# Kernel optimization log

Hardware: AMD Instinct MI355X
Metric: run time of the kernel (lower is better)

Reference implementation:

```python
import jax, jax.numpy as jnp
import numpy as np

EPS = 0.1
TANH_SCALE = 1.0
B, T, N, D, C, DE = 8, 120, 24, 48, 1128, 256  # C = D*(D-1)//2


def setup_inputs() -> dict:
    key = jax.random.key(0)
    k1, k2, k3, k4 = jax.random.split(key, 4)
    x = jax.random.normal(k1, (B, T, N, D), dtype=jnp.float32)
    context = jax.random.normal(k2, (B, C, N, DE), dtype=jnp.float32)
    Wkv = jax.random.normal(k3, (D, DE), dtype=jnp.float32) * (DE ** -0.5)
    bkv = jax.random.normal(k4, (D,), dtype=jnp.float32) * 0.01
    return {"x": x, "context": context, "Wkv": Wkv, "bkv": bkv}


def reference(x, context, Wkv, bkv):
    # x: [B,T,N,D], context: [B,C,N,DE]
    b, t, n, d = x.shape
    kv = jnp.einsum('bcne,de->bcnd', context, Wkv) + bkv      # [B,C,N,D]
    kv = jnp.transpose(kv, (0, 2, 3, 1))                      # [B,N,D,C]
    xt = jnp.transpose(x, (0, 2, 1, 3))                       # [B,N,T,D]
    sp = jnp.einsum('bntd,bndc->bntc', xt, kv)                # [B,N,T,C]
    sp = EPS * TANH_SCALE * jnp.tanh(sp / TANH_SCALE)
    i, j = jnp.tril_indices(d, k=-1)
    A = jnp.zeros((b, n, t, d, d), dtype=x.dtype).at[..., i, j].set(sp)
    A = A - jnp.swapaxes(A, -1, -2)                           # skew-symmetric
    dx = jnp.einsum('bntd,bntde->bnte', xt, A)                # per-(B,N,T) matvec
    y = xt + dx
    return jnp.transpose(y, (0, 2, 1, 3))                     # [B,T,N,D]
```

## Files before the change

kernel.cpp:

```cpp
#include <hip/hip_runtime.h>


constexpr int Bc = 8, Tc = 120, Nc = 24, Dc = 48, Cc = 1128, DEc = 256;
constexpr int BNc = Bc * Nc;
constexpr int KVP = 64;

using short8 = __attribute__((ext_vector_type(8))) short;
using f32x4  = __attribute__((ext_vector_type(4))) float;

__device__ __forceinline__ ushort f2b(float f) {
    union { float f; unsigned u; } v; v.f = f;
    unsigned r = (v.u + 0x7fffu + ((v.u >> 16) & 1u)) >> 16;
    return (ushort)r;
}
__device__ __forceinline__ short8 pack8(const float4& a, const float4& b) {
    short8 r;
    r[0] = (short)f2b(a.x); r[1] = (short)f2b(a.y); r[2] = (short)f2b(a.z); r[3] = (short)f2b(a.w);
    r[4] = (short)f2b(b.x); r[5] = (short)f2b(b.y); r[6] = (short)f2b(b.z); r[7] = (short)f2b(b.w);
    return r;
}

constexpr int SWs = 264;
constexpr int STs = 72;
__global__ __launch_bounds__(256) void k1_kv(const float* __restrict__ ctx,
                                             const float* __restrict__ Wkv,
                                             const float* __restrict__ bkv,
                                             ushort* __restrict__ kvb) {
    __shared__ ushort sW[Dc * SWs];
    __shared__ ushort sT[4][32 * STs];
    const int bn = blockIdx.x, c0 = blockIdx.y * 128;
    const int b = bn / Nc, n = bn % Nc;
    const int tid = threadIdx.x, wave = tid >> 6, lane = tid & 63;
    const int tr = lane & 15, kg = lane >> 4;
    const float* ctxb = ctx + ((size_t)b * Cc * Nc + n) * DEc;

    for (int l = tid; l < Dc * 64; l += 256) {
        int d = l >> 6, e4 = (l & 63) << 2;
        float4 w = *reinterpret_cast<const float4*>(Wkv + d * DEc + e4);
        ushort4 u = make_ushort4(f2b(w.x), f2b(w.y), f2b(w.z), f2b(w.w));
        *reinterpret_cast<ushort4*>(&sW[d * SWs + e4]) = u;
    }
    __syncthreads();

    const float* arow[2];
    #pragma unroll
    for (int mf = 0; mf < 2; ++mf) {
        int c = c0 + wave * 32 + mf * 16 + tr;
        arow[mf] = ctxb + (size_t)(c < Cc ? c : Cc - 1) * (Nc * DEc);
    }

    f32x4 acc[2][3];
    #pragma unroll
    for (int mf = 0; mf < 2; ++mf)
        #pragma unroll
        for (int nf = 0; nf < 3; ++nf) acc[mf][nf] = (f32x4){0.f, 0.f, 0.f, 0.f};

    #pragma unroll
    for (int ks = 0; ks < 8; ++ks) {
        const int e0 = ks * 32 + kg * 8;
        short8 af[2];
        #pragma unroll
        for (int mf = 0; mf < 2; ++mf) {
            float4 a0 = *reinterpret_cast<const float4*>(arow[mf] + e0);
            float4 a1 = *reinterpret_cast<const float4*>(arow[mf] + e0 + 4);
            af[mf] = pack8(a0, a1);
        }
        short8 bf[3];
        #pragma unroll
        for (int nf = 0; nf < 3; ++nf)
            bf[nf] = *reinterpret_cast<const short8*>(&sW[(nf * 16 + tr) * SWs + ks * 32 + kg * 8]);
        #pragma unroll
        for (int mf = 0; mf < 2; ++mf)
            #pragma unroll
            for (int nf = 0; nf < 3; ++nf)
                acc[mf][nf] = __builtin_amdgcn_mfma_f32_16x16x32_bf16(af[mf], bf[nf], acc[mf][nf], 0, 0, 0);
    }

    float bias[3];
    #pragma unroll
    for (int nf = 0; nf < 3; ++nf) bias[nf] = bkv[nf * 16 + tr];
    #pragma unroll
    for (int mf = 0; mf < 2; ++mf)
        #pragma unroll
        for (int nf = 0; nf < 3; ++nf)
            #pragma unroll
            for (int r = 0; r < 4; ++r)
                sT[wave][(mf * 16 + kg * 4 + r) * STs + nf * 16 + tr] = f2b(acc[mf][nf][r] + bias[nf]);
    {
        int row = lane >> 1, half = lane & 1;
        short8 z = (short8){0, 0, 0, 0, 0, 0, 0, 0};
        *reinterpret_cast<short8*>(&sT[wave][row * STs + 48 + half * 8]) = z;
    }
    __syncthreads();
    #pragma unroll
    for (int p = 0; p < 4; ++p) {
        int row = p * 8 + (lane >> 3), colv = (lane & 7) * 8;
        short8 v = *reinterpret_cast<const short8*>(&sT[wave][row * STs + colv]);
        int c = c0 + wave * 32 + row;
        if (c < Cc)
            *reinterpret_cast<short8*>(&kvb[((size_t)bn * Cc + c) * KVP + colv]) = v;
    }
}

constexpr int SGs = 1136;
__global__ __launch_bounds__(256) void k2_fused(const float* __restrict__ x,
                                                const ushort* __restrict__ kvb,
                                                float* __restrict__ out) {
    __shared__ float  sG[16 * SGs];
    __shared__ float  sXf[16 * 52];
    __shared__ ushort sXb[16 * 72];
    const int L = blockIdx.x;
    const int bn = (L & 7) + 8 * (L >> 6);
    const int tt = (L >> 3) & 7;
    const int b = bn / Nc, n = bn % Nc, t0 = tt * 16;
    const int tid = threadIdx.x, wave = tid >> 6, lane = tid & 63;
    const int tr = lane & 15, kg = lane >> 4;

    for (int l = tid; l < 16 * 72 / 4; l += 256)
        *reinterpret_cast<ushort4*>(&sXb[l * 4]) = make_ushort4(0, 0, 0, 0);
    __syncthreads();
    if (tid < 192) {
        int t = tid / 12, dv = (tid % 12) * 4, tg = t0 + t;
        float4 v = make_float4(0.f, 0.f, 0.f, 0.f);
        if (tg < Tc) v = *reinterpret_cast<const float4*>(x + (((size_t)b * Tc + tg) * Nc + n) * Dc + dv);
        *reinterpret_cast<float4*>(&sXf[t * 52 + dv]) = v;
        *reinterpret_cast<ushort4*>(&sXb[t * 72 + dv]) = make_ushort4(f2b(v.x), f2b(v.y), f2b(v.z), f2b(v.w));
    }
    __syncthreads();
    const short8 af0 = *reinterpret_cast<const short8*>(&sXb[tr * 72 + kg * 8]);
    const short8 af1 = *reinterpret_cast<const short8*>(&sXb[tr * 72 + 32 + kg * 8]);
    const ushort* kvbn = kvb + (size_t)bn * Cc * KVP;
    for (int nf = wave; nf < 71; nf += 4) {
        int c = nf * 16 + tr;
        int ce = c < Cc ? c : Cc - 1;
        short8 b0 = *reinterpret_cast<const short8*>(&kvbn[(size_t)ce * KVP + kg * 8]);
        short8 b1 = *reinterpret_cast<const short8*>(&kvbn[(size_t)ce * KVP + 32 + kg * 8]);
        f32x4 a = (f32x4){0.f, 0.f, 0.f, 0.f};
        a = __builtin_amdgcn_mfma_f32_16x16x32_bf16(af0, b0, a, 0, 0, 0);
        a = __builtin_amdgcn_mfma_f32_16x16x32_bf16(af1, b1, a, 0, 0, 0);
        #pragma unroll
        for (int r = 0; r < 4; ++r) {
            float g = 0.1f - 0.2f * __builtin_amdgcn_rcpf(__expf(2.0f * a[r]) + 1.0f);
            sG[(kg * 4 + r) * SGs + c] = g;
        }
    }
    __syncthreads();
    int ea[3], ta[3], tea[3];
    float dxa[3];
    #pragma unroll
    for (int p = 0; p < 3; ++p) {
        int idx = tid + p * 256;
        ta[p] = idx / 48; ea[p] = idx % 48;
        tea[p] = ea[p] * (ea[p] - 1) / 2;
        dxa[p] = 0.f;
    }
    int td = 0;
    #pragma unroll 4
    for (int d = 0; d < 48; ++d) {
        #pragma unroll
        for (int p = 0; p < 3; ++p) {
            bool gt = d > ea[p];
            int c = gt ? (td + ea[p]) : (tea[p] + d);
            float gv = sG[ta[p] * SGs + c];
            float xv = sXf[ta[p] * 52 + d];
            float m = gt ? xv : -xv;
            if (d == ea[p]) m = 0.f;
            dxa[p] = fmaf(m, gv, dxa[p]);
        }
        td += d;
    }
    #pragma unroll
    for (int p = 0; p < 3; ++p) {
        int tg = t0 + ta[p];
        if (tg < Tc)
            out[(((size_t)b * Tc + tg) * Nc + n) * Dc + ea[p]] = sXf[ta[p] * 52 + ea[p]] + dxa[p];
    }
}

extern "C" void kernel_launch(void* const* d_in, const int* in_sizes, int n_in,
                              void* d_out, int out_size, void* d_ws, size_t ws_size,
                              hipStream_t stream) {
    (void)in_sizes; (void)n_in; (void)out_size; (void)ws_size;
    const float* x   = (const float*)d_in[0];
    const float* ctx = (const float*)d_in[1];
    const float* Wkv = (const float*)d_in[2];
    const float* bkv = (const float*)d_in[3];
    float* out   = (float*)d_out;
    ushort* kvb  = (ushort*)d_ws;

    k1_kv<<<dim3(BNc, 9), dim3(256), 0, stream>>>(ctx, Wkv, bkv, kvb);
    k2_fused<<<dim3(BNc * 8), dim3(256), 0, stream>>>(x, kvb, out);
}
```

Before: 98.36 us.

## Fuse kv projection and skew matvec into one kernel via reassociated X·W product

Replaces the two-kernel pipeline with a single 1024-thread kernel per (b,n). It reassociates the product by first computing X·W^T (120x256) and then multiplying by the context, so kv is never materialised in global memory, and it folds the bias into a per-row x·bkv term. Eight waves produce tanh gates in 64-column chunks into a double-buffered LDS tile, while the other eight waves consume each chunk for the skew-symmetric matvec. In exchange, only 192 blocks are launched, each with a large LDS footprint, which can limit occupancy and parallelism. The gate values are now stored as bf16.

```diff
diff --git a/kernel.cpp b/kernel.cpp
--- a/kernel.cpp
+++ b/kernel.cpp
@@ -1,9 +1,9 @@
 #include <hip/hip_runtime.h>
+#include <hip/hip_bf16.h>
 
 
 constexpr int Bc = 8, Tc = 120, Nc = 24, Dc = 48, Cc = 1128, DEc = 256;
 constexpr int BNc = Bc * Nc;
-constexpr int KVP = 64;
 
 using short8 = __attribute__((ext_vector_type(8))) short;
 using f32x4  = __attribute__((ext_vector_type(4))) float;
@@ -12,6 +12,9 @@
     union { float f; unsigned u; } v; v.f = f;
     unsigned r = (v.u + 0x7fffu + ((v.u >> 16) & 1u)) >> 16;
     return (ushort)r;
+}
+__device__ __forceinline__ float b2f(ushort u) {
+    union { unsigned q; float f; } cv; cv.q = ((unsigned)u) << 16; return cv.f;
 }
 __device__ __forceinline__ short8 pack8(const float4& a, const float4& b) {
     short8 r;
@@ -20,174 +23,183 @@
     return r;
 }
 
-constexpr int SWs = 264;
-constexpr int STs = 72;
-__global__ __launch_bounds__(256) void k1_kv(const float* __restrict__ ctx,
-                                             const float* __restrict__ Wkv,
-                                             const float* __restrict__ bkv,
-                                             ushort* __restrict__ kvb) {
-    __shared__ ushort sW[Dc * SWs];
-    __shared__ ushort sT[4][32 * STs];
-    const int bn = blockIdx.x, c0 = blockIdx.y * 128;
-    const int b = bn / Nc, n = bn % Nc;
+constexpr int WTs = 64;
+constexpr int XFs = 52;
+constexpr int XWs = 264;
+constexpr int GSs = 74;
+constexpr int XBs = 72;
+constexpr int NCH = 18;
+
+__global__ __launch_bounds__(1024, 4) void k2f(const float* __restrict__ x,
+                                               const float* __restrict__ ctx,
+                                               const float* __restrict__ Wkv,
+                                               const float* __restrict__ bkv,
+                                               float* __restrict__ out) {
+    __shared__ ushort sWT[256 * WTs];
+    __shared__ float  sXf[Tc * XFs];
+    __shared__ ushort sXW[128 * XWs];
+    __shared__ ushort sG[2][128 * GSs];
+    ushort* sXb = &sG[0][0];
+
+    const int bn = blockIdx.x, b = bn / Nc, n = bn % Nc;
     const int tid = threadIdx.x, wave = tid >> 6, lane = tid & 63;
     const int tr = lane & 15, kg = lane >> 4;
     const float* ctxb = ctx + ((size_t)b * Cc * Nc + n) * DEc;
-
-    for (int l = tid; l < Dc * 64; l += 256) {
-        int d = l >> 6, e4 = (l & 63) << 2;
-        float4 w = *reinterpret_cast<const float4*>(Wkv + d * DEc + e4);
-        ushort4 u = make_ushort4(f2b(w.x), f2b(w.y), f2b(w.z), f2b(w.w));
-        *reinterpret_cast<ushort4*>(&sW[d * SWs + e4]) = u;
+    const float* xb   = x + ((size_t)b * Tc * Nc + n) * Dc;
+
+    for (int l = tid; l < 128 * XBs / 8; l += 1024)
+        *reinterpret_cast<short8*>(&sXb[l * 8]) = (short8){0, 0, 0, 0, 0, 0, 0, 0};
+    {
+        int e = tid >> 2, q = tid & 3;
+        *reinterpret_cast<ushort4*>(&sWT[e * WTs + 48 + q * 4]) = make_ushort4(0, 0, 0, 0);
+    }
+    for (int l = tid; l < Dc * DEc; l += 1024) {
+        int d = l >> 8, e = l & 255;
+        sWT[e * WTs + d] = f2b(Wkv[l]);
     }
     __syncthreads();
-
-    const float* arow[2];
-    #pragma unroll
-    for (int mf = 0; mf < 2; ++mf) {
-        int c = c0 + wave * 32 + mf * 16 + tr;
-        arow[mf] = ctxb + (size_t)(c < Cc ? c : Cc - 1) * (Nc * DEc);
-    }
-
-    f32x4 acc[2][3];
-    #pragma unroll
-    for (int mf = 0; mf < 2; ++mf)
+    for (int l = tid; l < Tc * 12; l += 1024) {
+        int t = l / 12, dv = (l % 12) * 4;
+        float4 v = *reinterpret_cast<const float4*>(xb + (size_t)t * Nc * Dc + dv);
+        *reinterpret_cast<float4*>(&sXf[t * XFs + dv]) = v;
+        *reinterpret_cast<ushort4*>(&sXb[t * XBs + dv]) =
+            make_ushort4(f2b(v.x), f2b(v.y), f2b(v.z), f2b(v.w));
+    }
+    __syncthreads();
+    if (tid < Tc) {
+        float a = 0.f;
+        for (int d = 0; d < Dc; ++d) a += sXf[tid * XFs + d] * bkv[d];
+        sXf[tid * XFs + 48] = a;
+    }
+    {
+        int m = wave & 7, nb = (wave >> 3) * 8;
+        short8 a0 = *reinterpret_cast<const short8*>(&sXb[(m * 16 + tr) * XBs + kg * 8]);
+        short8 a1 = *reinterpret_cast<const short8*>(&sXb[(m * 16 + tr) * XBs + 32 + kg * 8]);
         #pragma unroll
-        for (int nf = 0; nf < 3; ++nf) acc[mf][nf] = (f32x4){0.f, 0.f, 0.f, 0.f};
-
-    #pragma unroll
-    for (int ks = 0; ks < 8; ++ks) {
-        const int e0 = ks * 32 + kg * 8;
-        short8 af[2];
-        #pragma unroll
-        for (int mf = 0; mf < 2; ++mf) {
-            float4 a0 = *reinterpret_cast<const float4*>(arow[mf] + e0);
-            float4 a1 = *reinterpret_cast<const float4*>(arow[mf] + e0 + 4);
-            af[mf] = pack8(a0, a1);
-        }
-        short8 bf[3];
-        #pragma unroll
-        for (int nf = 0; nf < 3; ++nf)
-            bf[nf] = *reinterpret_cast<const short8*>(&sW[(nf * 16 + tr) * SWs + ks * 32 + kg * 8]);
-        #pragma unroll
-        for (int mf = 0; mf < 2; ++mf)
-            #pragma unroll
-            for (int nf = 0; nf < 3; ++nf)
-                acc[mf][nf] = __builtin_amdgcn_mfma_f32_16x16x32_bf16(af[mf], bf[nf], acc[mf][nf], 0, 0, 0);
-    }
-
-    float bias[3];
-    #pragma unroll
-    for (int nf = 0; nf < 3; ++nf) bias[nf] = bkv[nf * 16 + tr];
-    #pragma unroll
-    for (int mf = 0; mf < 2; ++mf)
-        #pragma unroll
-        for (int nf = 0; nf < 3; ++nf)
+        for (int j = 0; j < 8; ++j) {
+            int nf = nb + j;
+            short8 b0 = *reinterpret_cast<const short8*>(&sWT[(nf * 16 + tr) * WTs + kg * 8]);
+            short8 b1 = *reinterpret_cast<const short8*>(&sWT[(nf * 16 + tr) * WTs + 32 + kg * 8]);
+            f32x4 acc = (f32x4){0.f, 0.f, 0.f, 0.f};
+            acc = __builtin_amdgcn_mfma_f32_16x16x32_bf16(a0, b0, acc, 0, 0, 0);
+            acc = __builtin_amdgcn_mfma_f32_16x16x32_bf16(a1, b1, acc, 0, 0, 0);
             #pragma unroll
             for (int r = 0; r < 4; ++r)
-                sT[wave][(mf * 16 + kg * 4 + r) * STs + nf * 16 + tr] = f2b(acc[mf][nf][r] + bias[nf]);
-    {
-        int row = lane >> 1, half = lane & 1;
-        short8 z = (short8){0, 0, 0, 0, 0, 0, 0, 0};
-        *reinterpret_cast<short8*>(&sT[wave][row * STs + 48 + half * 8]) = z;
+                sXW[(m * 16 + kg * 4 + r) * XWs + nf * 16 + tr] = f2b(acc[r]);
+        }
     }
     __syncthreads();
-    #pragma unroll
-    for (int p = 0; p < 4; ++p) {
-        int row = p * 8 + (lane >> 3), colv = (lane & 7) * 8;
-        short8 v = *reinterpret_cast<const short8*>(&sT[wave][row * STs + colv]);
-        int c = c0 + wave * 32 + row;
-        if (c < Cc)
-            *reinterpret_cast<short8*>(&kvb[((size_t)bn * Cc + c) * KVP + colv]) = v;
-    }
-}
-
-constexpr int SGs = 1136;
-__global__ __launch_bounds__(256) void k2_fused(const float* __restrict__ x,
-                                                const ushort* __restrict__ kvb,
-                                                float* __restrict__ out) {
-    __shared__ float  sG[16 * SGs];
-    __shared__ float  sXf[16 * 52];
-    __shared__ ushort sXb[16 * 72];
-    const int L = blockIdx.x;
-    const int bn = (L & 7) + 8 * (L >> 6);
-    const int tt = (L >> 3) & 7;
-    const int b = bn / Nc, n = bn % Nc, t0 = tt * 16;
-    const int tid = threadIdx.x, wave = tid >> 6, lane = tid & 63;
-    const int tr = lane & 15, kg = lane >> 4;
-
-    for (int l = tid; l < 16 * 72 / 4; l += 256)
-        *reinterpret_cast<ushort4*>(&sXb[l * 4]) = make_ushort4(0, 0, 0, 0);
-    __syncthreads();
-    if (tid < 192) {
-        int t = tid / 12, dv = (tid % 12) * 4, tg = t0 + t;
-        float4 v = make_float4(0.f, 0.f, 0.f, 0.f);
-        if (tg < Tc) v = *reinterpret_cast<const float4*>(x + (((size_t)b * Tc + tg) * Nc + n) * Dc + dv);
-        *reinterpret_cast<float4*>(&sXf[t * 52 + dv]) = v;
-        *reinterpret_cast<ushort4*>(&sXb[t * 72 + dv]) = make_ushort4(f2b(v.x), f2b(v.y), f2b(v.z), f2b(v.w));
-    }
-    __syncthreads();
-    const short8 af0 = *reinterpret_cast<const short8*>(&sXb[tr * 72 + kg * 8]);
-    const short8 af1 = *reinterpret_cast<const short8*>(&sXb[tr * 72 + 32 + kg * 8]);
-    const ushort* kvbn = kvb + (size_t)bn * Cc * KVP;
-    for (int nf = wave; nf < 71; nf += 4) {
-        int c = nf * 16 + tr;
-        int ce = c < Cc ? c : Cc - 1;
-        short8 b0 = *reinterpret_cast<const short8*>(&kvbn[(size_t)ce * KVP + kg * 8]);
-        short8 b1 = *reinterpret_cast<const short8*>(&kvbn[(size_t)ce * KVP + 32 + kg * 8]);
-        f32x4 a = (f32x4){0.f, 0.f, 0.f, 0.f};
-        a = __builtin_amdgcn_mfma_f32_16x16x32_bf16(af0, b0, a, 0, 0, 0);
-        a = __builtin_amdgcn_mfma_f32_16x16x32_bf16(af1, b1, a, 0, 0, 0);
+
+    if (wave < 8) {
+        const int mq = wave & 3, nq = wave >> 2;
+        const ushort* arow0 = &sXW[(mq * 16 + tr) * XWs];
+        const ushort* arow1 = &sXW[((mq + 4) * 16 + tr) * XWs];
+        for (int ch = 0; ch < NCH + 1; ++ch) {
+            if (ch < NCH) {
+                int g0 = ch * 4 + 2 * nq, g1 = g0 + 1;
+                int ca = g0 * 16 + tr; if (ca > Cc - 1) ca = Cc - 1;
+                int cb = g1 * 16 + tr; if (cb > Cc - 1) cb = Cc - 1;
+                const float* pa = ctxb + (size_t)ca * (Nc * DEc) + kg * 8;
+                const float* pb = ctxb + (size_t)cb * (Nc * DEc) + kg * 8;
+                f32x4 acc[2][2];
+                #pragma unroll
+                for (int mi = 0; mi < 2; ++mi)
+                    #pragma unroll
+                    for (int ni = 0; ni < 2; ++ni) acc[mi][ni] = (f32x4){0.f, 0.f, 0.f, 0.f};
+                float4 fa0 = *reinterpret_cast<const float4*>(pa);
+                float4 fa1 = *reinterpret_cast<const float4*>(pa + 4);
+                float4 fb0 = *reinterpret_cast<const float4*>(pb);
+                float4 fb1 = *reinterpret_cast<const float4*>(pb + 4);
+                #pragma unroll
+                for (int ks = 0; ks < 8; ++ks) {
+                    float4 na0, na1, nb0, nb1;
+                    if (ks < 7) {
+                        na0 = *reinterpret_cast<const float4*>(pa + (ks + 1) * 32);
+                        na1 = *reinterpret_cast<const float4*>(pa + (ks + 1) * 32 + 4);
+                        nb0 = *reinterpret_cast<const float4*>(pb + (ks + 1) * 32);
+                        nb1 = *reinterpret_cast<const float4*>(pb + (ks + 1) * 32 + 4);
+                    }
+                    short8 bf0 = pack8(fa0, fa1), bf1 = pack8(fb0, fb1);
+                    short8 af0 = *reinterpret_cast<const short8*>(arow0 + ks * 32 + kg * 8);
+                    short8 af1 = *reinterpret_cast<const short8*>(arow1 + ks * 32 + kg * 8);
+                    acc[0][0] = __builtin_amdgcn_mfma_f32_16x16x32_bf16(af0, bf0, acc[0][0], 0, 0, 0);
+                    acc[0][1] = __builtin_amdgcn_mfma_f32_16x16x32_bf16(af0, bf1, acc[0][1], 0, 0, 0);
+                    acc[1][0] = __builtin_amdgcn_mfma_f32_16x16x32_bf16(af1, bf0, acc[1][0], 0, 0, 0);
+                    acc[1][1] = __builtin_amdgcn_mfma_f32_16x16x32_bf16(af1, bf1, acc[1][1], 0, 0, 0);
+                    fa0 = na0; fa1 = na1; fb0 = nb0; fb1 = nb1;
+                }
+                ushort* gb = &sG[ch & 1][0];
+                int lc0 = 2 * nq * 16 + tr, lc1 = lc0 + 16;
+                #pragma unroll
+                for (int mi = 0; mi < 2; ++mi) {
+                    int trow = (mq + mi * 4) * 16 + kg * 4;
+                    #pragma unroll
+                    for (int r = 0; r < 4; ++r) {
+                        int ts = trow + r; if (ts > Tc - 1) ts = Tc - 1;
+                        float sb = sXf[ts * XFs + 48];
+                        float s0 = acc[mi][0][r] + sb, s1 = acc[mi][1][r] + sb;
+                        float gv0 = 0.1f - 0.2f * __builtin_amdgcn_rcpf(__expf(2.f * s0) + 1.f);
+                        float gv1 = 0.1f - 0.2f * __builtin_amdgcn_rcpf(__expf(2.f * s1) + 1.f);
+                        gb[(trow + r) * GSs + lc0] = f2b(gv0);
+                        gb[(trow + r) * GSs + lc1] = f2b(gv1);
+                    }
+                }
+            }
+            __syncthreads();
+        }
+    } else {
+        const int ct = tid - 512;
+        const int tB = ct >> 2, eg = ct & 3;
+        const bool act = tB < Tc;
+        const float* xrow = &sXf[tB * XFs];
+        float dx[12]; int ii[12], Tv[12], Te[12];
         #pragma unroll
-        for (int r = 0; r < 4; ++r) {
-            float g = 0.1f - 0.2f * __builtin_amdgcn_rcpf(__expf(2.0f * a[r]) + 1.0f);
-            sG[(kg * 4 + r) * SGs + c] = g;
-        }
-    }
-    __syncthreads();
-    int ea[3], ta[3], tea[3];
-    float dxa[3];
-    #pragma unroll
-    for (int p = 0; p < 3; ++p) {
-        int idx = tid + p * 256;
-        ta[p] = idx / 48; ea[p] = idx % 48;
-        tea[p] = ea[p] * (ea[p] - 1) / 2;
-        dxa[p] = 0.f;
-    }
-    int td = 0;
-    #pragma unroll 4
-    for (int d = 0; d < 48; ++d) {
-        #pragma unroll
-        for (int p = 0; p < 3; ++p) {
-            bool gt = d > ea[p];
-            int c = gt ? (td + ea[p]) : (tea[p] + d);
-            float gv = sG[ta[p] * SGs + c];
-            float xv = sXf[ta[p] * 52 + d];
-            float m = gt ? xv : -xv;
-            if (d == ea[p]) m = 0.f;
-            dxa[p] = fmaf(m, gv, dxa[p]);
-        }
-        td += d;
-    }
-    #pragma unroll
-    for (int p = 0; p < 3; ++p) {
-        int tg = t0 + ta[p];
-        if (tg < Tc)
-            out[(((size_t)b * Tc + tg) * Nc + n) * Dc + ea[p]] = sXf[ta[p] * 52 + ea[p]] + dxa[p];
+        for (int p = 0; p < 12; ++p) {
+            int e = eg + 4 * p;
+            Te[p] = e * (e - 1) / 2;
+            ii[p] = e + 1;
+            Tv[p] = (e + 1) * e / 2;
+            dx[p] = 0.f;
+        }
+        for (int ch = 0; ch < NCH + 1; ++ch) {
+            if (ch > 0 && act) {
+                const int c0 = (ch - 1) * 64, c1 = c0 + 64;
+                const ushort* grow = &sG[(ch - 1) & 1][tB * GSs];
+                #pragma unroll
+                for (int p = 0; p < 12; ++p) {
+                    int e = eg + 4 * p;
+                    int jlo = c0 - Te[p]; if (jlo < 0) jlo = 0;
+                    int jhi = c1 - Te[p]; if (jhi > e) jhi = e;
+                    for (int j = jlo; j < jhi; ++j)
+                        dx[p] -= xrow[j] * b2f(grow[Te[p] + j - c0]);
+                    while (ii[p] < Dc && Tv[p] + e < c1) {
+                        dx[p] += xrow[ii[p]] * b2f(grow[Tv[p] + e - c0]);
+                        Tv[p] += ii[p]; ++ii[p];
+                    }
+                }
+            }
+            __syncthreads();
+        }
+        if (act) {
+            float* orow = out + (((size_t)b * Tc + tB) * Nc + n) * Dc;
+            #pragma unroll
+            for (int p = 0; p < 12; ++p) {
+                int e = eg + 4 * p;
+                orow[e] = sXf[tB * XFs + e] + dx[p];
+            }
+        }
     }
 }
 
 extern "C" void kernel_launch(void* const* d_in, const int* in_sizes, int n_in,
                               void* d_out, int out_size, void* d_ws, size_t ws_size,
                               hipStream_t stream) {
-    (void)in_sizes; (void)n_in; (void)out_size; (void)ws_size;
+    (void)in_sizes; (void)n_in; (void)out_size; (void)d_ws; (void)ws_size;
     const float* x   = (const float*)d_in[0];
     const float* ctx = (const float*)d_in[1];
     const float* Wkv = (const float*)d_in[2];
     const float* bkv = (const float*)d_in[3];
-    float* out   = (float*)d_out;
-    ushort* kvb  = (ushort*)d_ws;
-
-    k1_kv<<<dim3(BNc, 9), dim3(256), 0, stream>>>(ctx, Wkv, bkv, kvb);
-    k2_fused<<<dim3(BNc * 8), dim3(256), 0, stream>>>(x, kvb, out);
-}
+    float* out = (float*)d_out;
+
+    k2f<<<dim3(BNc), dim3(1024), 0, stream>>>(x, ctx, Wkv, bkv, out);
+}
```

Measured after the change: 161.1 us. 1.64x slower.
